# Kernel tuning notes

Measured on AMD Instinct MI355X. Metric: run time of the kernel, lower is better.

The kernel has to match this reference:

```python
import jax, jax.numpy as jnp
import numpy as np

N, E = 50000, 800000          # nodes, edges
F_IN, H, C = 32, 64, 7        # input feats, hidden, classes
EPS = 1e-5                    # BatchNorm eps


def setup_inputs() -> dict:
    key = jax.random.key(0)
    ks = jax.random.split(key, 16)
    inp = {
        "x": jax.random.normal(ks[0], (N, F_IN), jnp.float32),
        "edge_index": jax.random.randint(ks[1], (2, E), 0, N),
        "edge_attr": jax.random.uniform(ks[2], (E, 1), jnp.float32),
    }

    def conv_params(k, cin, cout, i):
        k1, k2 = jax.random.split(k)
        s = 1.0 / np.sqrt(cin)
        inp[f"W{i}"] = jax.random.uniform(k1, (2, cin, cout), jnp.float32, -s, s)  # spline kernel weights
        inp[f"R{i}"] = jax.random.uniform(k2, (cin, cout), jnp.float32, -s, s)     # root weight
        inp[f"B{i}"] = jnp.zeros((cout,), jnp.float32)

    conv_params(ks[3], F_IN, H, 0)
    conv_params(ks[4], H, H, 1)
    conv_params(ks[5], H, C, 2)
    for i in range(2):  # BatchNorm (eval mode: running stats)
        inp[f"G{i}"] = jnp.ones((H,), jnp.float32)
        inp[f"BE{i}"] = jnp.zeros((H,), jnp.float32)
        inp[f"RM{i}"] = 0.1 * jax.random.normal(ks[6 + 2 * i], (H,), jnp.float32)
        inp[f"RV{i}"] = jax.random.uniform(ks[7 + 2 * i], (H,), jnp.float32, 0.5, 1.5)
    return inp


def spline_conv(x, src, dst, u, W, R, B):
    # dim=1, kernel_size=2, degree=1 open B-spline:
    # basis = (1-u, u) with weight indices (0, 1) for u in [0,1).
    basis = jnp.stack([1.0 - u, u], axis=1)               # [E, 2]
    msg = jnp.einsum('ec,ek,kco->eo', x[src], basis, W)    # gather + basis-weighted linear
    agg = jax.ops.segment_sum(msg, dst, num_segments=N)    # scatter-add
    deg = jax.ops.segment_sum(jnp.ones((src.shape[0],), x.dtype), dst, num_segments=N)
    agg = agg / jnp.maximum(deg, 1.0)[:, None]             # aggr='mean' (default)
    return agg + x @ R + B                                 # root weight + bias


def batch_norm(x, g, b, rm, rv):
    return (x - rm) * jax.lax.rsqrt(rv + EPS) * g + b


def reference(x, edge_index, edge_attr,
              W0, R0, B0, W1, R1, B1, W2, R2, B2,
              G0, BE0, RM0, RV0, G1, BE1, RM1, RV1):
    src, dst = edge_index[0], edge_index[1]
    u = edge_attr[:, 0]
    h = spline_conv(x, src, dst, u, W0, R0, B0)
    h = jax.nn.elu(batch_norm(h, G0, BE0, RM0, RV0))
    h = spline_conv(h, src, dst, u, W1, R1, B1)
    h = jax.nn.elu(batch_norm(h, G1, BE1, RM1, RV1))
    h = spline_conv(h, src, dst, u, W2, R2, B2)
    return jax.nn.log_softmax(h, axis=1)
```

## Files before the change

kernel.cpp:

```cpp
#include <hip/hip_runtime.h>
#include <hip/hip_fp16.h>
#include <math.h>

#define NN 50000
#define NE 800000
#define EPSV 1e-5f
#define BSHIFT 7
#define BSIZE 128
#define NB 391
#define CAP 2560

typedef _Float16 h2f   __attribute__((ext_vector_type(2)));
typedef _Float16 f16x8 __attribute__((ext_vector_type(8)));
typedef float    f32x4 __attribute__((ext_vector_type(4)));

__global__ __launch_bounds__(64) void prep_all_kernel(
        const float* __restrict__ W0, const float* __restrict__ R0,
        const float* __restrict__ W1, const float* __restrict__ R1,
        const float* __restrict__ W2, const float* __restrict__ R2,
        const float* __restrict__ B0, const float* __restrict__ B1,
        const float* __restrict__ G0, const float* __restrict__ BE0,
        const float* __restrict__ RM0, const float* __restrict__ RV0,
        const float* __restrict__ G1, const float* __restrict__ BE1,
        const float* __restrict__ RM1, const float* __restrict__ RV1,
        __half* __restrict__ Bf0, __half* __restrict__ Bf1, __half* __restrict__ Bf7,
        float* __restrict__ bn0, float* __restrict__ bn1,
        int* __restrict__ bcursor) {
    int lane = threadIdx.x;
    int bid = blockIdx.x;
    int c = lane & 15;
    int kbase = ((lane >> 4) << 3);
    _Float16 vals[8];
    if (bid < 12) {
        int ks = bid >> 2, nt = bid & 3;
        int n = nt * 16 + c;
#pragma unroll
        for (int j = 0; j < 8; ++j) {
            int kg = ks * 32 + kbase + j;
            float v = (kg < 64) ? W0[(kg & 1) * 2048 + (kg >> 1) * 64 + n]
                                : R0[(kg - 64) * 64 + n];
            vals[j] = (_Float16)v;
        }
        *reinterpret_cast<f16x8*>(Bf0 + ((size_t)(bid * 64 + lane)) * 8) =
            *reinterpret_cast<f16x8*>(vals);
    } else if (bid < 36) {
        int t = bid - 12;
        int ks = t >> 2, nt = t & 3;
        int n = nt * 16 + c;
#pragma unroll
        for (int j = 0; j < 8; ++j) {
            int kg = ks * 32 + kbase + j;
            float v = (kg < 128) ? W1[(kg & 1) * 4096 + (kg >> 1) * 64 + n]
                                 : R1[(kg - 128) * 64 + n];
            vals[j] = (_Float16)v;
        }
        *reinterpret_cast<f16x8*>(Bf1 + ((size_t)(t * 64 + lane)) * 8) =
            *reinterpret_cast<f16x8*>(vals);
    } else if (bid < 40) {
        int ksnt = bid - 36;
        int ks = ksnt >> 1, nt = ksnt & 1;
#pragma unroll
        for (int j = 0; j < 8; ++j) {
            int k = ks * 32 + kbase + j;
            float v = 0.f;
            if (nt == 0) {
                if (c < 7)                 v = W2[k * 7 + c];
                else if (c >= 8 && c < 15) v = W2[448 + k * 7 + (c - 8)];
            } else {
                if (c < 7)                 v = R2[k * 7 + c];
            }
            vals[j] = (_Float16)v;
        }
        *reinterpret_cast<f16x8*>(Bf7 + ((size_t)(ksnt * 64 + lane)) * 8) =
            *reinterpret_cast<f16x8*>(vals);
    } else if (bid == 40) {
        float s = G0[lane] * rsqrtf(RV0[lane] + EPSV);
        bn0[lane] = s;
        bn0[64 + lane] = B0[lane] * s + BE0[lane] - RM0[lane] * s;
    } else if (bid == 41) {
        float s = G1[lane] * rsqrtf(RV1[lane] + EPSV);
        bn1[lane] = s;
        bn1[64 + lane] = B1[lane] * s + BE1[lane] - RM1[lane] * s;
    } else {
        int b = (bid - 42) * 64 + lane;
        if (b < NB) bcursor[b] = b * CAP;
    }
}

__global__ __launch_bounds__(256) void binB_xh_kernel(
        const int* __restrict__ src, const int* __restrict__ dst,
        const float* __restrict__ attr, int* __restrict__ bcursor,
        unsigned* __restrict__ es1su, unsigned char* __restrict__ es1dl, int E,
        const float* __restrict__ x, __half* __restrict__ xh) {
    __shared__ int hist[NB];
    __shared__ int base[NB];
    if (blockIdx.x >= NB) {
        int t = (blockIdx.x - NB) * 256 + threadIdx.x;
        size_t idx = (size_t)t * 8;
        if (idx < (size_t)NN * 32) {
            float4 f0 = *reinterpret_cast<const float4*>(x + idx);
            float4 f1 = *reinterpret_cast<const float4*>(x + idx + 4);
            _Float16 v[8] = {(_Float16)f0.x, (_Float16)f0.y, (_Float16)f0.z, (_Float16)f0.w,
                             (_Float16)f1.x, (_Float16)f1.y, (_Float16)f1.z, (_Float16)f1.w};
            *reinterpret_cast<f16x8*>(xh + idx) = *reinterpret_cast<f16x8*>(v);
        }
        return;
    }
    for (int i = threadIdx.x; i < NB; i += blockDim.x) hist[i] = 0;
    __syncthreads();
    const int chunk = (E + NB - 1) / NB;
    int e0 = blockIdx.x * chunk;
    int e1 = e0 + chunk; if (e1 > E) e1 = E;
    unsigned su[8]; unsigned char dlv[8]; short bv[8];
#pragma unroll
    for (int j = 0; j < 8; ++j) {
        int e = e0 + threadIdx.x + j * 256;
        if (e < e1) {
            int d = dst[e];
            int b = d >> BSHIFT;
            __half uh = __float2half_rn(attr[e]);
            su[j]  = ((unsigned)src[e] << 16) | (unsigned)__half_as_ushort(uh);
            dlv[j] = (unsigned char)(d & (BSIZE - 1));
            bv[j]  = (short)b;
            atomicAdd(&hist[b], 1);
        }
    }
    __syncthreads();
    for (int i = threadIdx.x; i < NB; i += blockDim.x) {
        int cnt = hist[i];
        base[i] = cnt ? atomicAdd(&bcursor[i], cnt) : 0;
        hist[i] = 0;
    }
    __syncthreads();
#pragma unroll
    for (int j = 0; j < 8; ++j) {
        int e = e0 + threadIdx.x + j * 256;
        if (e < e1) {
            int b = bv[j];
            int slot = base[b] + atomicAdd(&hist[b], 1);
            es1su[slot] = su[j];
            es1dl[slot] = dlv[j];
        }
    }
}

__global__ __launch_bounds__(256) void placeC_kernel(const int* __restrict__ bcursor,
                                                     const unsigned* __restrict__ es1su,
                                                     const unsigned char* __restrict__ es1dl,
                                                     int2* __restrict__ rowrange,
                                                     uint2* __restrict__ es8) {
    __shared__ int hist[BSIZE];
    __shared__ int stmp[BSIZE];
    __shared__ int cur[BSIZE];
    int b = blockIdx.x;
    int t = threadIdx.x;
    int bs = b * CAP;
    int be = bcursor[b];
    if (t < BSIZE) hist[t] = 0;
    __syncthreads();
    unsigned su[10]; unsigned char dlv[10];
#pragma unroll
    for (int j = 0; j < 10; ++j) {
        int i = bs + t + j * 256;
        if (i < be) {
            su[j]  = es1su[i];
            dlv[j] = es1dl[i];
            atomicAdd(&hist[dlv[j]], 1);
        }
    }
    __syncthreads();
    if (t < BSIZE) {
        int v = hist[t];
        int incl = v;
#pragma unroll
        for (int o = 1; o < 64; o <<= 1) {
            int nv = __shfl_up(incl, o, 64);
            if ((t & 63) >= o) incl += nv;
        }
        stmp[t] = incl;
    }
    __syncthreads();
    if (t < BSIZE) {
        int excl = stmp[t] - hist[t] + ((t >= 64) ? stmp[63] : 0);
        cur[t] = excl;
        int node = b * BSIZE + t;
        if (node < NN) {
            int2 rr; rr.x = bs + excl; rr.y = bs + excl + hist[t];
            rowrange[node] = rr;
        }
    }
    __syncthreads();
#pragma unroll
    for (int j = 0; j < 10; ++j) {
        int i = bs + t + j * 256;
        if (i < be) {
            unsigned r = su[j];
            int dl = dlv[j];
            int slot = bs + atomicAdd(&cur[dl], 1);
            __half uh = __ushort_as_half((unsigned short)(r & 0xffffu));
            __half2 p = __halves2half2(__hsub(__ushort_as_half((unsigned short)0x3C00u), uh), uh);
            uint2 rec;
            rec.x = r >> 16;
            rec.y = *reinterpret_cast<unsigned*>(&p);
            es8[slot] = rec;
        }
    }
}

__global__ __launch_bounds__(256, 8) void gatherS32_kernel(const int2* __restrict__ rowrange,
                                                           const uint2* __restrict__ es8,
                                                           const __half* __restrict__ xh,
                                                           __half* __restrict__ S, int n_nodes) {
    int n = (blockIdx.x * blockDim.x + threadIdx.x) >> 6;
    int lane = threadIdx.x & 63;
    if (n >= n_nodes) return;
    int2 rr = rowrange[n];
    int beg = __builtin_amdgcn_readfirstlane(rr.x);
    int end = __builtin_amdgcn_readfirstlane(rr.y);
    const unsigned c2 = (unsigned)((lane & 31) << 1);
    const char* xb = (const char*)xh;
    float a0 = 0.f, a1 = 0.f, a2 = 0.f, a3 = 0.f;
    float a4 = 0.f, a5 = 0.f, a6 = 0.f, a7 = 0.f;
    float b0 = 0.f, b1 = 0.f, b2 = 0.f, b3 = 0.f;
    float b4 = 0.f, b5 = 0.f, b6 = 0.f, b7 = 0.f;
    int i = beg + (lane >> 5);
    for (; i + 14 < end; i += 16) {
        uint2 q0 = es8[i];
        uint2 q1 = es8[i + 2];
        uint2 q2 = es8[i + 4];
        uint2 q3 = es8[i + 6];
        uint2 q4 = es8[i + 8];
        uint2 q5 = es8[i + 10];
        uint2 q6 = es8[i + 12];
        uint2 q7 = es8[i + 14];
        __half x0 = *(const __half*)(xb + ((q0.x << 6) | c2));
        __half x1 = *(const __half*)(xb + ((q1.x << 6) | c2));
        __half x2 = *(const __half*)(xb + ((q2.x << 6) | c2));
        __half x3 = *(const __half*)(xb + ((q3.x << 6) | c2));
        __half x4 = *(const __half*)(xb + ((q4.x << 6) | c2));
        __half x5 = *(const __half*)(xb + ((q5.x << 6) | c2));
        __half x6 = *(const __half*)(xb + ((q6.x << 6) | c2));
        __half x7 = *(const __half*)(xb + ((q7.x << 6) | c2));
        __half2 u0 = __builtin_bit_cast(__half2, q0.y);
        __half2 u1 = __builtin_bit_cast(__half2, q1.y);
        __half2 u2 = __builtin_bit_cast(__half2, q2.y);
        __half2 u3 = __builtin_bit_cast(__half2, q3.y);
        __half2 u4 = __builtin_bit_cast(__half2, q4.y);
        __half2 u5 = __builtin_bit_cast(__half2, q5.y);
        __half2 u6 = __builtin_bit_cast(__half2, q6.y);
        __half2 u7 = __builtin_bit_cast(__half2, q7.y);
        float f0 = __half2float(x0), f1 = __half2float(x1);
        float f2 = __half2float(x2), f3 = __half2float(x3);
        float f4 = __half2float(x4), f5 = __half2float(x5);
        float f6 = __half2float(x6), f7 = __half2float(x7);
        a0 = fmaf(__low2float(u0), f0, a0); b0 = fmaf(__high2float(u0), f0, b0);
        a1 = fmaf(__low2float(u1), f1, a1); b1 = fmaf(__high2float(u1), f1, b1);
        a2 = fmaf(__low2float(u2), f2, a2); b2 = fmaf(__high2float(u2), f2, b2);
        a3 = fmaf(__low2float(u3), f3, a3); b3 = fmaf(__high2float(u3), f3, b3);
        a4 = fmaf(__low2float(u4), f4, a4); b4 = fmaf(__high2float(u4), f4, b4);
        a5 = fmaf(__low2float(u5), f5, a5); b5 = fmaf(__high2float(u5), f5, b5);
        a6 = fmaf(__low2float(u6), f6, a6); b6 = fmaf(__high2float(u6), f6, b6);
        a7 = fmaf(__low2float(u7), f7, a7); b7 = fmaf(__high2float(u7), f7, b7);
    }
    for (; i < end; i += 2) {
        uint2 q = es8[i];
        float xv = __half2float(*(const __half*)(xb + ((q.x << 6) | c2)));
        __half2 u = __builtin_bit_cast(__half2, q.y);
        a0 = fmaf(__low2float(u), xv, a0); b0 = fmaf(__high2float(u), xv, b0);
    }
    float a = ((a0 + a1) + (a2 + a3)) + ((a4 + a5) + (a6 + a7));
    float b = ((b0 + b1) + (b2 + b3)) + ((b4 + b5) + (b6 + b7));
    a += __shfl_xor(a, 32);
    b += __shfl_xor(b, 32);
    float degv = (float)(end - beg);
    if (degv < 1.f) degv = 1.f;
    float inv = 1.f / degv;
    if (lane < 32) {
        reinterpret_cast<__half2*>(S + (size_t)n * 64)[lane] = __floats2half2_rn(a * inv, b * inv);
    }
}

__global__ __launch_bounds__(256, 8) void gatherS64_kernel(const int2* __restrict__ rowrange,
                                                           const uint2* __restrict__ es8,
                                                           const __half* __restrict__ ht,
                                                           __half* __restrict__ S, int n_nodes) {
    int n = (blockIdx.x * blockDim.x + threadIdx.x) >> 6;
    int lane = threadIdx.x & 63;
    if (n >= n_nodes) return;
    int2 rr = rowrange[n];
    int beg = __builtin_amdgcn_readfirstlane(rr.x);
    int end = __builtin_amdgcn_readfirstlane(rr.y);
    const unsigned c2 = (unsigned)(lane << 1);
    const char* xb = (const char*)ht;
    float a0 = 0.f, a1 = 0.f, a2 = 0.f, a3 = 0.f;
    float b0 = 0.f, b1 = 0.f, b2 = 0.f, b3 = 0.f;
    int i = beg;
    if (i < end && (i & 1)) {
        uint2 q = es8[i];
        float xv = __half2float(*(const __half*)(xb + ((q.x << 7) | c2)));
        __half2 u = __builtin_bit_cast(__half2, q.y);
        a0 = fmaf(__low2float(u), xv, a0); b0 = fmaf(__high2float(u), xv, b0);
        ++i;
    }
    for (; i + 7 < end; i += 8) {
        uint4 p0 = *reinterpret_cast<const uint4*>(es8 + i);
        uint4 p1 = *reinterpret_cast<const uint4*>(es8 + i + 2);
        uint4 p2 = *reinterpret_cast<const uint4*>(es8 + i + 4);
        uint4 p3 = *reinterpret_cast<const uint4*>(es8 + i + 6);
        __half x0 = *(const __half*)(xb + ((p0.x << 7) | c2));
        __half x1 = *(const __half*)(xb + ((p0.z << 7) | c2));
        __half x2 = *(const __half*)(xb + ((p1.x << 7) | c2));
        __half x3 = *(const __half*)(xb + ((p1.z << 7) | c2));
        __half x4 = *(const __half*)(xb + ((p2.x << 7) | c2));
        __half x5 = *(const __half*)(xb + ((p2.z << 7) | c2));
        __half x6 = *(const __half*)(xb + ((p3.x << 7) | c2));
        __half x7 = *(const __half*)(xb + ((p3.z << 7) | c2));
        __half2 u0 = __builtin_bit_cast(__half2, p0.y);
        __half2 u1 = __builtin_bit_cast(__half2, p0.w);
        __half2 u2 = __builtin_bit_cast(__half2, p1.y);
        __half2 u3 = __builtin_bit_cast(__half2, p1.w);
        __half2 u4 = __builtin_bit_cast(__half2, p2.y);
        __half2 u5 = __builtin_bit_cast(__half2, p2.w);
        __half2 u6 = __builtin_bit_cast(__half2, p3.y);
        __half2 u7 = __builtin_bit_cast(__half2, p3.w);
        float f0 = __half2float(x0), f1 = __half2float(x1);
        float f2 = __half2float(x2), f3 = __half2float(x3);
        float f4 = __half2float(x4), f5 = __half2float(x5);
        float f6 = __half2float(x6), f7 = __half2float(x7);
        a0 = fmaf(__low2float(u0), f0, a0); b0 = fmaf(__high2float(u0), f0, b0);
        a1 = fmaf(__low2float(u1), f1, a1); b1 = fmaf(__high2float(u1), f1, b1);
        a2 = fmaf(__low2float(u2), f2, a2); b2 = fmaf(__high2float(u2), f2, b2);
        a3 = fmaf(__low2float(u3), f3, a3); b3 = fmaf(__high2float(u3), f3, b3);
        a0 = fmaf(__low2float(u4), f4, a0); b0 = fmaf(__high2float(u4), f4, b0);
        a1 = fmaf(__low2float(u5), f5, a1); b1 = fmaf(__high2float(u5), f5, b1);
        a2 = fmaf(__low2float(u6), f6, a2); b2 = fmaf(__high2float(u6), f6, b2);
        a3 = fmaf(__low2float(u7), f7, a3); b3 = fmaf(__high2float(u7), f7, b3);
    }
    for (; i + 1 < end; i += 2) {
        uint4 p = *reinterpret_cast<const uint4*>(es8 + i);
        float f0 = __half2float(*(const __half*)(xb + ((p.x << 7) | c2)));
        float f1 = __half2float(*(const __half*)(xb + ((p.z << 7) | c2)));
        __half2 u0 = __builtin_bit_cast(__half2, p.y);
        __half2 u1 = __builtin_bit_cast(__half2, p.w);
        a0 = fmaf(__low2float(u0), f0, a0); b0 = fmaf(__high2float(u0), f0, b0);
        a1 = fmaf(__low2float(u1), f1, a1); b1 = fmaf(__high2float(u1), f1, b1);
    }
    if (i < end) {
        uint2 q = es8[i];
        float xv = __half2float(*(const __half*)(xb + ((q.x << 7) | c2)));
        __half2 u = __builtin_bit_cast(__half2, q.y);
        a0 = fmaf(__low2float(u), xv, a0); b0 = fmaf(__high2float(u), xv, b0);
    }
    float a = (a0 + a1) + (a2 + a3);
    float b = (b0 + b1) + (b2 + b3);
    float degv = (float)(end - beg);
    if (degv < 1.f) degv = 1.f;
    float inv = 1.f / degv;
    reinterpret_cast<__half2*>(S + (size_t)n * 128)[lane] = __floats2half2_rn(a * inv, b * inv);
}

__global__ __launch_bounds__(256) void gemmL0_kernel(const __half* __restrict__ S,
                                                     const __half* __restrict__ xh,
                                                     const __half* __restrict__ Bf0,
                                                     const float* __restrict__ bn,
                                                     __half* __restrict__ hout, int n_nodes) {
    const int lane = threadIdx.x & 63;
    const int wid  = threadIdx.x >> 6;
    int m0 = (blockIdx.x * 4 + wid) * 16;
    if (m0 >= n_nodes) return;
    f32x4 acc[4];
#pragma unroll
    for (int i = 0; i < 4; ++i) acc[i] = (f32x4){0.f, 0.f, 0.f, 0.f};
    const int arow = m0 + (lane & 15);
    const int koff = ((lane >> 4) << 3);
    const f16x8* bf = reinterpret_cast<const f16x8*>(Bf0);
    const _Float16* sp = (const _Float16*)S  + (size_t)arow * 64 + koff;
    const _Float16* xp = (const _Float16*)xh + (size_t)arow * 32 + koff;
    f16x8 a0 = *reinterpret_cast<const f16x8*>(sp);
    f16x8 a1 = *reinterpret_cast<const f16x8*>(sp + 32);
    f16x8 a2 = *reinterpret_cast<const f16x8*>(xp);
#pragma unroll
    for (int nt = 0; nt < 4; ++nt)
        acc[nt] = __builtin_amdgcn_mfma_f32_16x16x32_f16(a0, bf[nt * 64 + lane], acc[nt], 0, 0, 0);
#pragma unroll
    for (int nt = 0; nt < 4; ++nt)
        acc[nt] = __builtin_amdgcn_mfma_f32_16x16x32_f16(a1, bf[(4 + nt) * 64 + lane], acc[nt], 0, 0, 0);
#pragma unroll
    for (int nt = 0; nt < 4; ++nt)
        acc[nt] = __builtin_amdgcn_mfma_f32_16x16x32_f16(a2, bf[(8 + nt) * 64 + lane], acc[nt], 0, 0, 0);
    const int c_lo  = lane & 15;
    const int rbase = ((lane >> 4) << 2);
#pragma unroll
    for (int nt = 0; nt < 4; ++nt) {
        int cc = nt * 16 + c_lo;
        float sc = bn[cc], sh = bn[64 + cc];
#pragma unroll
        for (int r = 0; r < 4; ++r) {
            int row = m0 + rbase + r;
            if (row < n_nodes) {
                float v = acc[nt][r] * sc + sh;
                v = v > 0.f ? v : expm1f(v);
                hout[(size_t)row * 64 + cc] = __float2half(v);
            }
        }
    }
}

__global__ __launch_bounds__(256) void gemmL1_7_kernel(const __half* __restrict__ S,
                                                       const __half* __restrict__ hin,
                                                       const __half* __restrict__ Bf1,
                                                       const __half* __restrict__ Bf7,
                                                       const float* __restrict__ bn,
                                                       const float* __restrict__ Bb2,
                                                       __half* __restrict__ Yab7H,
                                                       float* __restrict__ Z7,
                                                       int n_nodes) {
    __shared__ __align__(16) char ldsH[64 * 128];
    const int lane = threadIdx.x & 63;
    const int wid  = threadIdx.x >> 6;
    int m0 = (blockIdx.x * 4 + wid) * 16;
    if (m0 >= n_nodes) return;
    f32x4 acc[4];
#pragma unroll
    for (int i = 0; i < 4; ++i) acc[i] = (f32x4){0.f, 0.f, 0.f, 0.f};
    const int arow = m0 + (lane & 15);
    const int g = lane >> 4;
    const int koff = g << 3;
    const f16x8* bf = reinterpret_cast<const f16x8*>(Bf1);
    const _Float16* sp = (const _Float16*)S   + (size_t)arow * 128 + koff;
    const _Float16* hp = (const _Float16*)hin + (size_t)arow * 64  + koff;
#pragma unroll
    for (int ks = 0; ks < 6; ++ks) {
        f16x8 av = (ks < 4) ? *reinterpret_cast<const f16x8*>(sp + ks * 32)
                            : *reinterpret_cast<const f16x8*>(hp + (ks - 4) * 32);
#pragma unroll
        for (int nt = 0; nt < 4; ++nt)
            acc[nt] = __builtin_amdgcn_mfma_f32_16x16x32_f16(av, bf[(ks * 4 + nt) * 64 + lane], acc[nt], 0, 0, 0);
    }
    const int c_lo  = lane & 15;
    const int rbase = ((lane >> 4) << 2);
#pragma unroll
    for (int nt = 0; nt < 4; ++nt) {
        int cc = nt * 16 + c_lo;
        float sc = bn[cc], sh = bn[64 + cc];
#pragma unroll
        for (int r = 0; r < 4; ++r) {
            float v = acc[nt][r] * sc + sh;
            v = v > 0.f ? v : expm1f(v);
            int rl = wid * 16 + rbase + r;
            *reinterpret_cast<__half*>(ldsH + ((rl * 128 + cc * 2) ^ ((rl & 7) << 4))) = __float2half(v);
        }
    }

    const int rowl = wid * 16 + (lane & 15);
    const int swz = (rowl & 7) << 4;
    f32x4 acc7[2];
    acc7[0] = (f32x4){0.f, 0.f, 0.f, 0.f};
    acc7[1] = (f32x4){0.f, 0.f, 0.f, 0.f};
    const f16x8* bf7 = reinterpret_cast<const f16x8*>(Bf7);
#pragma unroll
    for (int ks = 0; ks < 2; ++ks) {
        f16x8 av = *reinterpret_cast<const f16x8*>(ldsH + ((rowl * 128 + ks * 64 + g * 16) ^ swz));
#pragma unroll
        for (int nt = 0; nt < 2; ++nt)
            acc7[nt] = __builtin_amdgcn_mfma_f32_16x16x32_f16(av, bf7[(ks * 2 + nt) * 64 + lane], acc7[nt], 0, 0, 0);
    }
#pragma unroll
    for (int r = 0; r < 4; ++r) {
        int row = m0 + rbase + r;
        if (row < n_nodes) {
            if (c_lo < 7) {
                Yab7H[((size_t)row << 4) + 2 * c_lo] = __float2half(acc7[0][r]);
                Z7[((size_t)row << 3) + c_lo] = acc7[1][r] + Bb2[c_lo];
            } else if (c_lo >= 8 && c_lo < 15) {
                Yab7H[((size_t)row << 4) + 2 * (c_lo - 8) + 1] = __float2half(acc7[0][r]);
            }
        }
    }
}

__global__ void gather7_final_kernel(const int2* __restrict__ rowrange,
                                     const uint2* __restrict__ es8,
                                     const __half2* __restrict__ Yab7H,
                                     const float* __restrict__ Z7,
                                     float* __restrict__ out, int n_nodes) {
    int t = blockIdx.x * blockDim.x + threadIdx.x;
    int n = t >> 3;
    int c = t & 7;
    if (n >= n_nodes) return;
    int2 rr = rowrange[n];
    int beg = rr.x, end = rr.y;
    const unsigned c4 = (unsigned)(c << 2);
    const char* yb = (const char*)Yab7H;
    float acc0 = 0.f, acc1 = 0.f, acc2 = 0.f, acc3 = 0.f;
    if (c < 7) {
        int i = beg;
        for (; i + 7 < end; i += 8) {
            uint2 q0 = es8[i];
            uint2 q1 = es8[i + 1];
            uint2 q2 = es8[i + 2];
            uint2 q3 = es8[i + 3];
            uint2 q4 = es8[i + 4];
            uint2 q5 = es8[i + 5];
            uint2 q6 = es8[i + 6];
            uint2 q7 = es8[i + 7];
            __half2 v0 = *(const __half2*)(yb + ((q0.x << 5) | c4));
            __half2 v1 = *(const __half2*)(yb + ((q1.x << 5) | c4));
            __half2 v2 = *(const __half2*)(yb + ((q2.x << 5) | c4));
            __half2 v3 = *(const __half2*)(yb + ((q3.x << 5) | c4));
            __half2 v4 = *(const __half2*)(yb + ((q4.x << 5) | c4));
            __half2 v5 = *(const __half2*)(yb + ((q5.x << 5) | c4));
            __half2 v6 = *(const __half2*)(yb + ((q6.x << 5) | c4));
            __half2 v7 = *(const __half2*)(yb + ((q7.x << 5) | c4));
            acc0 = __builtin_amdgcn_fdot2(__builtin_bit_cast(h2f, v0), __builtin_bit_cast(h2f, q0.y), acc0, false);
            acc1 = __builtin_amdgcn_fdot2(__builtin_bit_cast(h2f, v1), __builtin_bit_cast(h2f, q1.y), acc1, false);
            acc2 = __builtin_amdgcn_fdot2(__builtin_bit_cast(h2f, v2), __builtin_bit_cast(h2f, q2.y), acc2, false);
            acc3 = __builtin_amdgcn_fdot2(__builtin_bit_cast(h2f, v3), __builtin_bit_cast(h2f, q3.y), acc3, false);
            acc0 = __builtin_amdgcn_fdot2(__builtin_bit_cast(h2f, v4), __builtin_bit_cast(h2f, q4.y), acc0, false);
            acc1 = __builtin_amdgcn_fdot2(__builtin_bit_cast(h2f, v5), __builtin_bit_cast(h2f, q5.y), acc1, false);
            acc2 = __builtin_amdgcn_fdot2(__builtin_bit_cast(h2f, v6), __builtin_bit_cast(h2f, q6.y), acc2, false);
            acc3 = __builtin_amdgcn_fdot2(__builtin_bit_cast(h2f, v7), __builtin_bit_cast(h2f, q7.y), acc3, false);
        }
        for (; i < end; ++i) {
            uint2 q = es8[i];
            __half2 v = *(const __half2*)(yb + ((q.x << 5) | c4));
            acc0 = __builtin_amdgcn_fdot2(__builtin_bit_cast(h2f, v), __builtin_bit_cast(h2f, q.y), acc0, false);
        }
    }
    float acc = (acc0 + acc1) + (acc2 + acc3);
    float degv = (float)(end - beg);
    if (degv < 1.f) degv = 1.f;
    float v = (c < 7) ? (acc / degv + Z7[(n << 3) + c]) : -1e30f;
    float m = v;
#pragma unroll
    for (int o = 1; o < 8; o <<= 1) m = fmaxf(m, __shfl_xor(m, o, 8));
    float ex = (c < 7) ? expf(v - m) : 0.f;
    float ssum = ex;
#pragma unroll
    for (int o = 1; o < 8; o <<= 1) ssum += __shfl_xor(ssum, o, 8);
    if (c < 7) out[n * 7 + c] = v - m - logf(ssum);
}

extern "C" void kernel_launch(void* const* d_in, const int* in_sizes, int n_in,
                              void* d_out, int out_size, void* d_ws, size_t ws_size,
                              hipStream_t stream) {
    const float* x    = (const float*)d_in[0];
    const int*   ei   = (const int*)d_in[1];
    const float* attr = (const float*)d_in[2];
    const float* W0 = (const float*)d_in[3];
    const float* R0 = (const float*)d_in[4];
    const float* B0 = (const float*)d_in[5];
    const float* W1 = (const float*)d_in[6];
    const float* R1 = (const float*)d_in[7];
    const float* B1 = (const float*)d_in[8];
    const float* W2 = (const float*)d_in[9];
    const float* R2 = (const float*)d_in[10];
    const float* B2 = (const float*)d_in[11];
    const float* G0  = (const float*)d_in[12];
    const float* BE0 = (const float*)d_in[13];
    const float* RM0 = (const float*)d_in[14];
    const float* RV0 = (const float*)d_in[15];
    const float* G1  = (const float*)d_in[16];
    const float* BE1 = (const float*)d_in[17];
    const float* RM1 = (const float*)d_in[18];
    const float* RV1 = (const float*)d_in[19];

    const int* src = ei;
    const int* dst = ei + NE;
    float* out = (float*)d_out;

    char* ws = (char*)d_ws;
    size_t off = 0;
    auto alloc = [&](size_t bytes) { char* p = ws + off; off += (bytes + 255) & ~size_t(255); return p; };
    int*           bcursor  = (int*)          alloc(NB * sizeof(int));
    int2*          rowrange = (int2*)         alloc((size_t)NN * sizeof(int2));
    unsigned*      es1su    = (unsigned*)     alloc((size_t)NB * CAP * sizeof(unsigned));
    unsigned char* es1dl    = (unsigned char*)alloc((size_t)NB * CAP * sizeof(unsigned char));
    uint2*         es8      = (uint2*)        alloc((size_t)NB * CAP * sizeof(uint2));
    __half*        Bf0      = (__half*)       alloc((size_t)12 * 64 * 8 * sizeof(__half));
    __half*        Bf1      = (__half*)       alloc((size_t)24 * 64 * 8 * sizeof(__half));
    __half*        Bf7      = (__half*)       alloc((size_t)4 * 64 * 8 * sizeof(__half));
    float*         bn0      = (float*)        alloc(128 * sizeof(float));
    float*         bn1      = (float*)        alloc(128 * sizeof(float));
    __half*        xh       = (__half*)       alloc((size_t)(NN + 64) * 32 * sizeof(__half));
    __half*        S        = (__half*)       alloc((size_t)(NN + 64) * 128 * sizeof(__half));
    __half*        h0       = (__half*)       alloc((size_t)(NN + 64) * 64 * sizeof(__half));
    __half*        Yab7H    = (__half*)       alloc((size_t)NN * 16 * sizeof(__half));
    float*         Z7       = (float*)        alloc((size_t)NN * 8 * sizeof(float));

    const int B = 256;
    const int gM    = ((NN + 15) / 16 + 3) / 4;
    const int gGath = (NN * 64) / B;
    const int gN8   = (NN * 8 + B - 1) / B;
    const int gConv = ((NN * 32 / 8) + B - 1) / B;
    const int gPrep = 42 + (NB + 63) / 64;

    prep_all_kernel<<<gPrep, 64, 0, stream>>>(W0, R0, W1, R1, W2, R2, B0, B1,
                                              G0, BE0, RM0, RV0, G1, BE1, RM1, RV1,
                                              Bf0, Bf1, Bf7, bn0, bn1, bcursor);

    binB_xh_kernel<<<NB + gConv, B, 0, stream>>>(src, dst, attr, bcursor, es1su, es1dl, NE, x, xh);

    placeC_kernel<<<NB, B, 0, stream>>>(bcursor, es1su, es1dl, rowrange, es8);

    gatherS32_kernel<<<gGath, B, 0, stream>>>(rowrange, es8, xh, S, NN);
    gemmL0_kernel<<<gM, B, 0, stream>>>(S, xh, Bf0, bn0, h0, NN);

    gatherS64_kernel<<<gGath, B, 0, stream>>>(rowrange, es8, h0, S, NN);
    gemmL1_7_kernel<<<gM, B, 0, stream>>>(S, h0, Bf1, Bf7, bn1, B2, Yab7H, Z7, NN);

    gather7_final_kernel<<<gN8, B, 0, stream>>>(rowrange, es8, (const __half2*)Yab7H, Z7, out, NN);
}
```

Before: 209.6 us.

## Split layer-1 features into two 32-wide planes gathered on separate XCD groups

The 64-wide hidden features from layer 0 are stored as two 32-column planes. The layer-1 gather is launched with twice as many blocks, and the block id is mapped so that XCDs 0-3 gather the low plane and XCDs 4-7 the high plane. Each XCD's L2 then only has to hold a 3.2 MB table instead of the full 6.4 MB, which is meant to raise L2 hit rates for the random row gathers. The cost is that edge records are read twice, each gather moves 64 bytes per row instead of 128, and the code assumes blocks are dispatched round-robin across the 8 XCDs.

```diff
diff --git a/kernel.cpp b/kernel.cpp
--- a/kernel.cpp
+++ b/kernel.cpp
@@ -207,18 +207,11 @@
     }
 }
 
-__global__ __launch_bounds__(256, 8) void gatherS32_kernel(const int2* __restrict__ rowrange,
-                                                           const uint2* __restrict__ es8,
-                                                           const __half* __restrict__ xh,
-                                                           __half* __restrict__ S, int n_nodes) {
-    int n = (blockIdx.x * blockDim.x + threadIdx.x) >> 6;
-    int lane = threadIdx.x & 63;
-    if (n >= n_nodes) return;
-    int2 rr = rowrange[n];
-    int beg = __builtin_amdgcn_readfirstlane(rr.x);
-    int end = __builtin_amdgcn_readfirstlane(rr.y);
+__device__ __forceinline__ void gather_plane_body(int beg, int end, int lane,
+                                                  const uint2* __restrict__ es8,
+                                                  const char* __restrict__ xb,
+                                                  __half2* __restrict__ Sout) {
     const unsigned c2 = (unsigned)((lane & 31) << 1);
-    const char* xb = (const char*)xh;
     float a0 = 0.f, a1 = 0.f, a2 = 0.f, a3 = 0.f;
     float a4 = 0.f, a5 = 0.f, a6 = 0.f, a7 = 0.f;
     float b0 = 0.f, b1 = 0.f, b2 = 0.f, b3 = 0.f;
@@ -276,13 +269,13 @@
     if (degv < 1.f) degv = 1.f;
     float inv = 1.f / degv;
     if (lane < 32) {
-        reinterpret_cast<__half2*>(S + (size_t)n * 64)[lane] = __floats2half2_rn(a * inv, b * inv);
-    }
-}
-
-__global__ __launch_bounds__(256, 8) void gatherS64_kernel(const int2* __restrict__ rowrange,
+        Sout[lane & 31] = __floats2half2_rn(a * inv, b * inv);
+    }
+}
+
+__global__ __launch_bounds__(256, 8) void gatherS32_kernel(const int2* __restrict__ rowrange,
                                                            const uint2* __restrict__ es8,
-                                                           const __half* __restrict__ ht,
+                                                           const __half* __restrict__ xh,
                                                            __half* __restrict__ S, int n_nodes) {
     int n = (blockIdx.x * blockDim.x + threadIdx.x) >> 6;
     int lane = threadIdx.x & 63;
@@ -290,80 +283,37 @@
     int2 rr = rowrange[n];
     int beg = __builtin_amdgcn_readfirstlane(rr.x);
     int end = __builtin_amdgcn_readfirstlane(rr.y);
-    const unsigned c2 = (unsigned)(lane << 1);
-    const char* xb = (const char*)ht;
-    float a0 = 0.f, a1 = 0.f, a2 = 0.f, a3 = 0.f;
-    float b0 = 0.f, b1 = 0.f, b2 = 0.f, b3 = 0.f;
-    int i = beg;
-    if (i < end && (i & 1)) {
-        uint2 q = es8[i];
-        float xv = __half2float(*(const __half*)(xb + ((q.x << 7) | c2)));
-        __half2 u = __builtin_bit_cast(__half2, q.y);
-        a0 = fmaf(__low2float(u), xv, a0); b0 = fmaf(__high2float(u), xv, b0);
-        ++i;
-    }
-    for (; i + 7 < end; i += 8) {
-        uint4 p0 = *reinterpret_cast<const uint4*>(es8 + i);
-        uint4 p1 = *reinterpret_cast<const uint4*>(es8 + i + 2);
-        uint4 p2 = *reinterpret_cast<const uint4*>(es8 + i + 4);
-        uint4 p3 = *reinterpret_cast<const uint4*>(es8 + i + 6);
-        __half x0 = *(const __half*)(xb + ((p0.x << 7) | c2));
-        __half x1 = *(const __half*)(xb + ((p0.z << 7) | c2));
-        __half x2 = *(const __half*)(xb + ((p1.x << 7) | c2));
-        __half x3 = *(const __half*)(xb + ((p1.z << 7) | c2));
-        __half x4 = *(const __half*)(xb + ((p2.x << 7) | c2));
-        __half x5 = *(const __half*)(xb + ((p2.z << 7) | c2));
-        __half x6 = *(const __half*)(xb + ((p3.x << 7) | c2));
-        __half x7 = *(const __half*)(xb + ((p3.z << 7) | c2));
-        __half2 u0 = __builtin_bit_cast(__half2, p0.y);
-        __half2 u1 = __builtin_bit_cast(__half2, p0.w);
-        __half2 u2 = __builtin_bit_cast(__half2, p1.y);
-        __half2 u3 = __builtin_bit_cast(__half2, p1.w);
-        __half2 u4 = __builtin_bit_cast(__half2, p2.y);
-        __half2 u5 = __builtin_bit_cast(__half2, p2.w);
-        __half2 u6 = __builtin_bit_cast(__half2, p3.y);
-        __half2 u7 = __builtin_bit_cast(__half2, p3.w);
-        float f0 = __half2float(x0), f1 = __half2float(x1);
-        float f2 = __half2float(x2), f3 = __half2float(x3);
-        float f4 = __half2float(x4), f5 = __half2float(x5);
-        float f6 = __half2float(x6), f7 = __half2float(x7);
-        a0 = fmaf(__low2float(u0), f0, a0); b0 = fmaf(__high2float(u0), f0, b0);
-        a1 = fmaf(__low2float(u1), f1, a1); b1 = fmaf(__high2float(u1), f1, b1);
-        a2 = fmaf(__low2float(u2), f2, a2); b2 = fmaf(__high2float(u2), f2, b2);
-        a3 = fmaf(__low2float(u3), f3, a3); b3 = fmaf(__high2float(u3), f3, b3);
-        a0 = fmaf(__low2float(u4), f4, a0); b0 = fmaf(__high2float(u4), f4, b0);
-        a1 = fmaf(__low2float(u5), f5, a1); b1 = fmaf(__high2float(u5), f5, b1);
-        a2 = fmaf(__low2float(u6), f6, a2); b2 = fmaf(__high2float(u6), f6, b2);
-        a3 = fmaf(__low2float(u7), f7, a3); b3 = fmaf(__high2float(u7), f7, b3);
-    }
-    for (; i + 1 < end; i += 2) {
-        uint4 p = *reinterpret_cast<const uint4*>(es8 + i);
-        float f0 = __half2float(*(const __half*)(xb + ((p.x << 7) | c2)));
-        float f1 = __half2float(*(const __half*)(xb + ((p.z << 7) | c2)));
-        __half2 u0 = __builtin_bit_cast(__half2, p.y);
-        __half2 u1 = __builtin_bit_cast(__half2, p.w);
-        a0 = fmaf(__low2float(u0), f0, a0); b0 = fmaf(__high2float(u0), f0, b0);
-        a1 = fmaf(__low2float(u1), f1, a1); b1 = fmaf(__high2float(u1), f1, b1);
-    }
-    if (i < end) {
-        uint2 q = es8[i];
-        float xv = __half2float(*(const __half*)(xb + ((q.x << 7) | c2)));
-        __half2 u = __builtin_bit_cast(__half2, q.y);
-        a0 = fmaf(__low2float(u), xv, a0); b0 = fmaf(__high2float(u), xv, b0);
-    }
-    float a = (a0 + a1) + (a2 + a3);
-    float b = (b0 + b1) + (b2 + b3);
-    float degv = (float)(end - beg);
-    if (degv < 1.f) degv = 1.f;
-    float inv = 1.f / degv;
-    reinterpret_cast<__half2*>(S + (size_t)n * 128)[lane] = __floats2half2_rn(a * inv, b * inv);
+    gather_plane_body(beg, end, lane, es8, (const char*)xh,
+                      reinterpret_cast<__half2*>(S + (size_t)n * 64));
+}
+
+__global__ __launch_bounds__(256, 8) void gatherP_kernel(const int2* __restrict__ rowrange,
+                                                         const uint2* __restrict__ es8,
+                                                         const __half* __restrict__ h0lo,
+                                                         const __half* __restrict__ h0hi,
+                                                         __half* __restrict__ S, int n_nodes) {
+    int bid = blockIdx.x;
+    int xcd = bid & 7;
+    int plane = xcd >> 2;
+    int ipb = (bid >> 3) * 4 + (xcd & 3);
+    int wid = threadIdx.x >> 6;
+    int lane = threadIdx.x & 63;
+    int n = ipb * 4 + wid;
+    if (n >= n_nodes) return;
+    int2 rr = rowrange[n];
+    int beg = __builtin_amdgcn_readfirstlane(rr.x);
+    int end = __builtin_amdgcn_readfirstlane(rr.y);
+    const char* table = (const char*)(plane ? h0hi : h0lo);
+    gather_plane_body(beg, end, lane, es8, table,
+                      reinterpret_cast<__half2*>(S + (size_t)n * 128 + plane * 64));
 }
 
 __global__ __launch_bounds__(256) void gemmL0_kernel(const __half* __restrict__ S,
                                                      const __half* __restrict__ xh,
                                                      const __half* __restrict__ Bf0,
                                                      const float* __restrict__ bn,
-                                                     __half* __restrict__ hout, int n_nodes) {
+                                                     __half* __restrict__ h0lo,
+                                                     __half* __restrict__ h0hi, int n_nodes) {
     const int lane = threadIdx.x & 63;
     const int wid  = threadIdx.x >> 6;
     int m0 = (blockIdx.x * 4 + wid) * 16;
@@ -393,6 +343,8 @@
 #pragma unroll
     for (int nt = 0; nt < 4; ++nt) {
         int cc = nt * 16 + c_lo;
+        __half* plane = (nt < 2) ? h0lo : h0hi;
+        int cp = cc & 31;
         float sc = bn[cc], sh = bn[64 + cc];
 #pragma unroll
         for (int r = 0; r < 4; ++r) {
@@ -400,14 +352,15 @@
             if (row < n_nodes) {
                 float v = acc[nt][r] * sc + sh;
                 v = v > 0.f ? v : expm1f(v);
-                hout[(size_t)row * 64 + cc] = __float2half(v);
+                plane[(size_t)row * 32 + cp] = __float2half(v);
             }
         }
     }
 }
 
 __global__ __launch_bounds__(256) void gemmL1_7_kernel(const __half* __restrict__ S,
-                                                       const __half* __restrict__ hin,
+                                                       const __half* __restrict__ h0lo,
+                                                       const __half* __restrict__ h0hi,
                                                        const __half* __restrict__ Bf1,
                                                        const __half* __restrict__ Bf7,
                                                        const float* __restrict__ bn,
@@ -427,12 +380,15 @@
     const int g = lane >> 4;
     const int koff = g << 3;
     const f16x8* bf = reinterpret_cast<const f16x8*>(Bf1);
-    const _Float16* sp = (const _Float16*)S   + (size_t)arow * 128 + koff;
-    const _Float16* hp = (const _Float16*)hin + (size_t)arow * 64  + koff;
+    const _Float16* sp  = (const _Float16*)S    + (size_t)arow * 128 + koff;
+    const _Float16* hpl = (const _Float16*)h0lo + (size_t)arow * 32  + koff;
+    const _Float16* hph = (const _Float16*)h0hi + (size_t)arow * 32  + koff;
 #pragma unroll
     for (int ks = 0; ks < 6; ++ks) {
-        f16x8 av = (ks < 4) ? *reinterpret_cast<const f16x8*>(sp + ks * 32)
-                            : *reinterpret_cast<const f16x8*>(hp + (ks - 4) * 32);
+        f16x8 av;
+        if (ks < 4)      av = *reinterpret_cast<const f16x8*>(sp + ks * 32);
+        else if (ks == 4) av = *reinterpret_cast<const f16x8*>(hpl);
+        else              av = *reinterpret_cast<const f16x8*>(hph);
 #pragma unroll
         for (int nt = 0; nt < 4; ++nt)
             acc[nt] = __builtin_amdgcn_mfma_f32_16x16x32_f16(av, bf[(ks * 4 + nt) * 64 + lane], acc[nt], 0, 0, 0);
@@ -584,16 +540,18 @@
     float*         bn1      = (float*)        alloc(128 * sizeof(float));
     __half*        xh       = (__half*)       alloc((size_t)(NN + 64) * 32 * sizeof(__half));
     __half*        S        = (__half*)       alloc((size_t)(NN + 64) * 128 * sizeof(__half));
-    __half*        h0       = (__half*)       alloc((size_t)(NN + 64) * 64 * sizeof(__half));
+    __half*        h0lo     = (__half*)       alloc((size_t)(NN + 64) * 32 * sizeof(__half));
+    __half*        h0hi     = (__half*)       alloc((size_t)(NN + 64) * 32 * sizeof(__half));
     __half*        Yab7H    = (__half*)       alloc((size_t)NN * 16 * sizeof(__half));
     float*         Z7       = (float*)        alloc((size_t)NN * 8 * sizeof(float));
 
     const int B = 256;
-    const int gM    = ((NN + 15) / 16 + 3) / 4;
-    const int gGath = (NN * 64) / B;
-    const int gN8   = (NN * 8 + B - 1) / B;
-    const int gConv = ((NN * 32 / 8) + B - 1) / B;
-    const int gPrep = 42 + (NB + 63) / 64;
+    const int gM     = ((NN + 15) / 16 + 3) / 4;
+    const int gGath  = (NN * 64) / B;
+    const int gGathP = 2 * gGath;
+    const int gN8    = (NN * 8 + B - 1) / B;
+    const int gConv  = ((NN * 32 / 8) + B - 1) / B;
+    const int gPrep  = 42 + (NB + 63) / 64;
 
     prep_all_kernel<<<gPrep, 64, 0, stream>>>(W0, R0, W1, R1, W2, R2, B0, B1,
                                               G0, BE0, RM0, RV0, G1, BE1, RM1, RV1,
@@ -604,10 +562,10 @@
     placeC_kernel<<<NB, B, 0, stream>>>(bcursor, es1su, es1dl, rowrange, es8);
 
     gatherS32_kernel<<<gGath, B, 0, stream>>>(rowrange, es8, xh, S, NN);
-    gemmL0_kernel<<<gM, B, 0, stream>>>(S, xh, Bf0, bn0, h0, NN);
-
-    gatherS64_kernel<<<gGath, B, 0, stream>>>(rowrange, es8, h0, S, NN);
-    gemmL1_7_kernel<<<gM, B, 0, stream>>>(S, h0, Bf1, Bf7, bn1, B2, Yab7H, Z7, NN);
+    gemmL0_kernel<<<gM, B, 0, stream>>>(S, xh, Bf0, bn0, h0lo, h0hi, NN);
+
+    gatherP_kernel<<<gGathP, B, 0, stream>>>(rowrange, es8, h0lo, h0hi, S, NN);
+    gemmL1_7_kernel<<<gM, B, 0, stream>>>(S, h0lo, h0hi, Bf1, Bf7, bn1, B2, Yab7H, Z7, NN);
 
     gather7_final_kernel<<<gN8, B, 0, stream>>>(rowrange, es8, (const __half2*)Yab7H, Z7, out, NN);
 }
```

Measured after the change: 245.8 us. 1.17x slower.

## Pad per-node edge lists to multiples of 16 and drop remainder loops

Applied to the files above, without the earlier changes.

The bucket sort now rounds each destination node's edge segment up to a multiple of 16 and fills the padding with zero records (source 0, zero basis weights). The true degree and the padded length are packed into rowrange.y. All three gather kernels loop only over full unrolled chunks, with no tail or alignment loops. This removes remainder handling and misaligned vector loads, but the kernels read and process extra padding edges. Bucket capacity is raised so the padded segments still fit.

```diff
diff --git a/kernel.cpp b/kernel.cpp
--- a/kernel.cpp
+++ b/kernel.cpp
@@ -8,7 +8,7 @@
 #define BSHIFT 7
 #define BSIZE 128
 #define NB 391
-#define CAP 2560
+#define CAP 3840
 
 typedef _Float16 h2f   __attribute__((ext_vector_type(2)));
 typedef _Float16 f16x8 __attribute__((ext_vector_type(8)));
@@ -171,7 +171,8 @@
     __syncthreads();
     if (t < BSIZE) {
         int v = hist[t];
-        int incl = v;
+        int pv = (v + 15) & ~15;
+        int incl = pv;
 #pragma unroll
         for (int o = 1; o < 64; o <<= 1) {
             int nv = __shfl_up(incl, o, 64);
@@ -181,11 +182,13 @@
     }
     __syncthreads();
     if (t < BSIZE) {
-        int excl = stmp[t] - hist[t] + ((t >= 64) ? stmp[63] : 0);
+        int v = hist[t];
+        int pv = (v + 15) & ~15;
+        int excl = stmp[t] - pv + ((t >= 64) ? stmp[63] : 0);
         cur[t] = excl;
         int node = b * BSIZE + t;
         if (node < NN) {
-            int2 rr; rr.x = bs + excl; rr.y = bs + excl + hist[t];
+            int2 rr; rr.x = bs + excl; rr.y = (v << 16) | pv;
             rowrange[node] = rr;
         }
     }
@@ -205,6 +208,15 @@
             es8[slot] = rec;
         }
     }
+    __syncthreads();
+    if (t < BSIZE) {
+        int v = hist[t];
+        int pv = (v + 15) & ~15;
+        int start = bs + cur[t];
+        int endp  = bs + (cur[t] - v) + pv;
+        uint2 z; z.x = 0u; z.y = 0u;
+        for (int k = start; k < endp; ++k) es8[k] = z;
+    }
 }
 
 __global__ __launch_bounds__(256, 8) void gatherS32_kernel(const int2* __restrict__ rowrange,
@@ -215,8 +227,9 @@
     int lane = threadIdx.x & 63;
     if (n >= n_nodes) return;
     int2 rr = rowrange[n];
-    int beg = __builtin_amdgcn_readfirstlane(rr.x);
-    int end = __builtin_amdgcn_readfirstlane(rr.y);
+    int beg  = __builtin_amdgcn_readfirstlane(rr.x);
+    int meta = __builtin_amdgcn_readfirstlane(rr.y);
+    int end = beg + (meta & 0xffff);
     const unsigned c2 = (unsigned)((lane & 31) << 1);
     const char* xb = (const char*)xh;
     float a0 = 0.f, a1 = 0.f, a2 = 0.f, a3 = 0.f;
@@ -262,21 +275,15 @@
         a6 = fmaf(__low2float(u6), f6, a6); b6 = fmaf(__high2float(u6), f6, b6);
         a7 = fmaf(__low2float(u7), f7, a7); b7 = fmaf(__high2float(u7), f7, b7);
     }
-    for (; i < end; i += 2) {
-        uint2 q = es8[i];
-        float xv = __half2float(*(const __half*)(xb + ((q.x << 6) | c2)));
-        __half2 u = __builtin_bit_cast(__half2, q.y);
-        a0 = fmaf(__low2float(u), xv, a0); b0 = fmaf(__high2float(u), xv, b0);
-    }
     float a = ((a0 + a1) + (a2 + a3)) + ((a4 + a5) + (a6 + a7));
     float b = ((b0 + b1) + (b2 + b3)) + ((b4 + b5) + (b6 + b7));
     a += __shfl_xor(a, 32);
     b += __shfl_xor(b, 32);
-    float degv = (float)(end - beg);
+    float degv = (float)(meta >> 16);
     if (degv < 1.f) degv = 1.f;
     float inv = 1.f / degv;
     if (lane < 32) {
-        reinterpret_cast<__half2*>(S + (size_t)n * 64)[lane] = __floats2half2_rn(a * inv, b * inv);
+        reinterpret_cast<__half2*>(S + (size_t)n * 64)[lane & 31] = __floats2half2_rn(a * inv, b * inv);
     }
 }
 
@@ -288,21 +295,14 @@
     int lane = threadIdx.x & 63;
     if (n >= n_nodes) return;
     int2 rr = rowrange[n];
-    int beg = __builtin_amdgcn_readfirstlane(rr.x);
-    int end = __builtin_amdgcn_readfirstlane(rr.y);
+    int beg  = __builtin_amdgcn_readfirstlane(rr.x);
+    int meta = __builtin_amdgcn_readfirstlane(rr.y);
+    int end = beg + (meta & 0xffff);
     const unsigned c2 = (unsigned)(lane << 1);
     const char* xb = (const char*)ht;
     float a0 = 0.f, a1 = 0.f, a2 = 0.f, a3 = 0.f;
     float b0 = 0.f, b1 = 0.f, b2 = 0.f, b3 = 0.f;
-    int i = beg;
-    if (i < end && (i & 1)) {
-        uint2 q = es8[i];
-        float xv = __half2float(*(const __half*)(xb + ((q.x << 7) | c2)));
-        __half2 u = __builtin_bit_cast(__half2, q.y);
-        a0 = fmaf(__low2float(u), xv, a0); b0 = fmaf(__high2float(u), xv, b0);
-        ++i;
-    }
-    for (; i + 7 < end; i += 8) {
+    for (int i = beg; i + 7 < end; i += 8) {
         uint4 p0 = *reinterpret_cast<const uint4*>(es8 + i);
         uint4 p1 = *reinterpret_cast<const uint4*>(es8 + i + 2);
         uint4 p2 = *reinterpret_cast<const uint4*>(es8 + i + 4);
@@ -336,24 +336,9 @@
         a2 = fmaf(__low2float(u6), f6, a2); b2 = fmaf(__high2float(u6), f6, b2);
         a3 = fmaf(__low2float(u7), f7, a3); b3 = fmaf(__high2float(u7), f7, b3);
     }
-    for (; i + 1 < end; i += 2) {
-        uint4 p = *reinterpret_cast<const uint4*>(es8 + i);
-        float f0 = __half2float(*(const __half*)(xb + ((p.x << 7) | c2)));
-        float f1 = __half2float(*(const __half*)(xb + ((p.z << 7) | c2)));
-        __half2 u0 = __builtin_bit_cast(__half2, p.y);
-        __half2 u1 = __builtin_bit_cast(__half2, p.w);
-        a0 = fmaf(__low2float(u0), f0, a0); b0 = fmaf(__high2float(u0), f0, b0);
-        a1 = fmaf(__low2float(u1), f1, a1); b1 = fmaf(__high2float(u1), f1, b1);
-    }
-    if (i < end) {
-        uint2 q = es8[i];
-        float xv = __half2float(*(const __half*)(xb + ((q.x << 7) | c2)));
-        __half2 u = __builtin_bit_cast(__half2, q.y);
-        a0 = fmaf(__low2float(u), xv, a0); b0 = fmaf(__high2float(u), xv, b0);
-    }
     float a = (a0 + a1) + (a2 + a3);
     float b = (b0 + b1) + (b2 + b3);
-    float degv = (float)(end - beg);
+    float degv = (float)(meta >> 16);
     if (degv < 1.f) degv = 1.f;
     float inv = 1.f / degv;
     reinterpret_cast<__half2*>(S + (size_t)n * 128)[lane] = __floats2half2_rn(a * inv, b * inv);
@@ -489,13 +474,13 @@
     int c = t & 7;
     if (n >= n_nodes) return;
     int2 rr = rowrange[n];
-    int beg = rr.x, end = rr.y;
+    int beg = rr.x;
+    int end = beg + (rr.y & 0xffff);
     const unsigned c4 = (unsigned)(c << 2);
     const char* yb = (const char*)Yab7H;
     float acc0 = 0.f, acc1 = 0.f, acc2 = 0.f, acc3 = 0.f;
     if (c < 7) {
-        int i = beg;
-        for (; i + 7 < end; i += 8) {
+        for (int i = beg; i + 7 < end; i += 8) {
             uint2 q0 = es8[i];
             uint2 q1 = es8[i + 1];
             uint2 q2 = es8[i + 2];
@@ -521,14 +506,9 @@
             acc2 = __builtin_amdgcn_fdot2(__builtin_bit_cast(h2f, v6), __builtin_bit_cast(h2f, q6.y), acc2, false);
             acc3 = __builtin_amdgcn_fdot2(__builtin_bit_cast(h2f, v7), __builtin_bit_cast(h2f, q7.y), acc3, false);
         }
-        for (; i < end; ++i) {
-            uint2 q = es8[i];
-            __half2 v = *(const __half2*)(yb + ((q.x << 5) | c4));
-            acc0 = __builtin_amdgcn_fdot2(__builtin_bit_cast(h2f, v), __builtin_bit_cast(h2f, q.y), acc0, false);
-        }
     }
     float acc = (acc0 + acc1) + (acc2 + acc3);
-    float degv = (float)(end - beg);
+    float degv = (float)(rr.y >> 16);
     if (degv < 1.f) degv = 1.f;
     float v = (c < 7) ? (acc / degv + Z7[(n << 3) + c]) : -1e30f;
     float m = v;
```

New measurement: 209.8 us. About the same (+0.1%).
